# Kernel tuning notes

Measured on AMD Instinct MI355X. Metric: run time of the kernel, lower is better.

The kernel has to match this reference:

```python
import jax, jax.numpy as jnp
import numpy as np

D = 2        # dof (input_dim of fc1)
H1 = 64      # hidden width
N = 262144   # batch
NEG_SLOPE = -0.01  # NOTE: original uses self.neg_slope=-0.01 in the analytic derivative
                   # while the forward activation uses F.leaky_relu default slope +0.01.
                   # We replicate this exactly.

def _lin_init(k, out_d, in_d):
    bound = 1.0 / np.sqrt(in_d)
    kw, kb = jax.random.split(k)
    W = jax.random.uniform(kw, (out_d, in_d), minval=-bound, maxval=bound, dtype=jnp.float32)
    b = jax.random.uniform(kb, (out_d,), minval=-bound, maxval=bound, dtype=jnp.float32)
    return W, b

def setup_inputs():
    key = jax.random.key(0)
    ks = jax.random.split(key, 6)
    W1, b1 = _lin_init(ks[0], H1, D)
    W1a, b1a = _lin_init(ks[1], H1, H1)
    W2, b2 = _lin_init(ks[2], D, H1)
    W3, b3 = _lin_init(ks[3], D, H1)
    W4, b4 = _lin_init(ks[4], 1, H1)
    x = jax.random.normal(ks[5], (N, 3 * D), dtype=jnp.float32)
    return {"x": x, "W1": W1, "b1": b1, "W1a": W1a, "b1a": b1a,
            "W2": W2, "b2": b2, "W3": W3, "b3": b3, "W4": W4, "b4": b4}

def _forward(x, W1, b1, W1a, b1a, W2, b2, W3, b3, W4, b4):
    n = x.shape[0]
    d = x.shape[1] // 3
    q, qd, qdd = x[:, :d], x[:, d:2 * d], x[:, 2 * d:]

    h1 = jax.nn.leaky_relu(q @ W1.T + b1, 0.01)       # [n,H1]
    h2 = jax.nn.leaky_relu(h1 @ W1a.T + b1a, 0.01)    # [n,H1]
    g = h2 @ W2.T + b2                                # [n,d]
    ld = jax.nn.relu(h2 @ W3.T + b3)                  # [n,d]  diagonal of L
    lo = h2 @ W4.T + b4                               # [n,1]  off-diagonal(s)

    # Analytic Jacobians. diag_embed(a) @ W == a[:,:,None] * W (no [n,H,H] materialization).
    dR1 = jnp.where(h1 > 0, 1.0, NEG_SLOPE)
    dh1_dq = dR1[:, :, None] * W1[None]                              # [n,H1,d]
    dR2 = jnp.where(h2 > 0, 1.0, NEG_SLOPE)
    dh2_dq = dR2[:, :, None] * jnp.einsum('hk,nkd->nhd', W1a, dh1_dq)  # [n,H1,d]
    dR3 = jnp.where(ld > 0, 1.0, 0.0)
    dld_dq = dR3[:, :, None] * jnp.einsum('oh,nhd->nod', W3, dh2_dq)   # [n,d,d]
    dlo_dq = jnp.einsum('oh,nhd->nod', W4, dh2_dq)                     # [n,1,d]

    dld_dqi = jnp.transpose(dld_dq, (0, 2, 1))[..., None]  # [n,d,d,1]
    dlo_dqi = jnp.transpose(dlo_dq, (0, 2, 1))[..., None]  # [n,d,1,1]
    dld_dt = dld_dq @ qd[:, :, None]                       # [n,d,1]
    dlo_dt = dlo_dq @ qd[:, :, None]                       # [n,1,1]

    zeros = jnp.zeros_like(ld)
    zeros2 = jnp.zeros_like(dld_dqi)
    Lc, dLt, dLq = [], [], []
    s, e = 0, d - 1
    for i in range(d):  # loop over d (=2) columns of the Cholesky factor
        Lc.append(jnp.concatenate([zeros[:, :i], ld[:, i:i + 1], lo[:, s:e]], axis=1))
        dLt.append(jnp.concatenate([zeros[:, :i], dld_dt[:, i].reshape(n, 1),
                                    dlo_dt[:, s:e].reshape(n, -1)], axis=1))
        dLq.append(jnp.concatenate([zeros2[:, :, :i].reshape(n, d, -1),
                                    dld_dqi[:, :, i].reshape(n, d, 1),
                                    dlo_dqi[:, :, s:e].reshape(n, d, -1)], axis=2))
        s, e = s + e, e + d - 2 - i
    L = jnp.stack(Lc, axis=2)                                    # [n,d,d]
    dL_dt = jnp.stack(dLt, axis=2)                               # [n,d,d]
    dL_dqi = jnp.transpose(jnp.stack(dLq, axis=3), (0, 2, 3, 1)) # [n,d,d,d]

    eps = 1e-5
    Lt = jnp.swapaxes(L, 1, 2)
    Hm = L @ Lt + eps * jnp.eye(d, dtype=x.dtype)
    dH_dt = L @ jnp.swapaxes(dL_dt, 1, 2) + dL_dt @ Lt

    qts = []
    for i in range(d):
        A = dL_dqi[..., i] @ Lt + L @ jnp.swapaxes(dL_dqi[..., i], 1, 2)
        qts.append(qd[:, None, :] @ A @ qd[:, :, None])  # [n,1,1]
    quad = jnp.stack(qts, axis=1).reshape(n, d, 1)

    c = dH_dt @ qd[:, :, None] - 0.5 * quad
    tau = Hm @ qdd[:, :, None] + c + g[:, :, None]
    return tau[..., 0], Hm, c[..., 0], g

def reference(x, W1, b1, W1a, b1a, W2, b2, W3, b3, W4, b4):
    return _forward(x, W1, b1, W1a, b1a, W2, b2, W3, b3, W4, b4)
```

## Files before the change

kernel.cpp:

```cpp
#include <hip/hip_runtime.h>
#include <stdint.h>


typedef __attribute__((ext_vector_type(8))) _Float16 f16x8;
typedef __attribute__((ext_vector_type(4))) float f32x4;
typedef __attribute__((ext_vector_type(2))) float f32x2;
typedef __attribute__((ext_vector_type(4))) unsigned int u32x4;

#define MFMA16(A,B,C) __builtin_amdgcn_mfma_f32_16x16x32_f16((A),(B),(C),0,0,0)

static __device__ __forceinline__ f32x2 pk_fma(f32x2 a, f32x2 b, f32x2 c) {
    f32x2 d;
    asm("v_pk_fma_f32 %0, %1, %2, %3" : "=v"(d) : "v"(a), "v"(b), "v"(c));
    return d;
}
static __device__ __forceinline__ f32x2 pk_mul(f32x2 a, f32x2 b) {
    f32x2 d;
    asm("v_pk_mul_f32 %0, %1, %2" : "=v"(d) : "v"(a), "v"(b));
    return d;
}
static __device__ __forceinline__ unsigned pkmul16(unsigned a, unsigned b) {
    unsigned d;
    asm("v_pk_mul_f16 %0, %1, %2" : "=v"(d) : "v"(a), "v"(b));
    return d;
}
static __device__ __forceinline__ float qsum(float v) {
    float a = v, b = v;
    asm("v_permlane16_swap_b32 %0, %1" : "+v"(a), "+v"(b));
    const float s = a + b;
    float c = s, d = s;
    asm("v_permlane32_swap_b32 %0, %1" : "+v"(c), "+v"(d));
    return c + d;
}

__global__ __launch_bounds__(256, 4) void delan_fwd(
    const float* __restrict__ x,
    const float* __restrict__ W1,  const float* __restrict__ b1,
    const float* __restrict__ W1a, const float* __restrict__ b1a,
    const float* __restrict__ W2,  const float* __restrict__ b2,
    const float* __restrict__ W3,  const float* __restrict__ b3,
    const float* __restrict__ W4,  const float* __restrict__ b4,
    float* __restrict__ out, int n_total)
{
    __shared__ _Float16 afrag[2][4][2][64][8];
    __shared__ float w0s[64], w1s[64], bs[64];
    __shared__ float cst[6][64];

    const int tid  = threadIdx.x;
    const int lane = tid & 63;
    const int wid  = tid >> 6;
    const int p    = lane & 15;
    const int qrt  = lane >> 4;
    const int s    = blockIdx.x * 64 + wid * 16 + p;
    const int sc   = (s < n_total) ? s : (n_total - 1);

    const float2 xa = *(const float2*)(x + 6 * sc);
    const float2 xb = *(const float2*)(x + 6 * sc + 2);
    const float2 xc = *(const float2*)(x + 6 * sc + 4);
    const float x0 = xa.x, x1 = xa.y;
    const float x2 = xb.x, x3 = xb.y;
    const float x4 = xc.x, x5 = xc.y;

    if (tid < 64) {
        const int k = tid;
        w0s[k] = W1[2*k]; w1s[k] = W1[2*k+1]; bs[k] = b1[k];
        cst[0][k] = W2[k];      cst[1][k] = W2[64 + k];
        cst[2][k] = W3[k];      cst[3][k] = W3[64 + k];
        cst[4][k] = W4[k];      cst[5][k] = b1a[k];
    }
    {
        const int ht = wid;
#pragma unroll
        for (int kh = 0; kh < 2; ++kh) {
            const int row = ht * 16 + p;
            const int kb  = kh * 32 + qrt * 8;
            float wv[8];
            *(float4*)&wv[0] = *(const float4*)(W1a + row * 64 + kb);
            *(float4*)&wv[4] = *(const float4*)(W1a + row * 64 + kb + 4);
            f16x8 hi, lo;
#pragma unroll
            for (int j = 0; j < 8; ++j) {
                const _Float16 h = (_Float16)wv[j];
                hi[j] = h;
                lo[j] = (_Float16)((wv[j] - (float)h) * 4096.0f);
            }
            *(f16x8*)&afrag[0][ht][kh][lane][0] = hi;
            *(f16x8*)&afrag[1][ht][kh][lane][0] = lo;
        }
    }
    __syncthreads();

    const f32x2 c4096  = {4096.0f, 4096.0f};
    const f32x2 cm4096 = {-4096.0f, -4096.0f};

    const f32x2 q00 = {x0, x0};
    const f32x2 q11 = {x1, x1};
    u32x4 Bhh[2], Bhl[2], Bu0[2], Bu1[2];
#pragma unroll
    for (int kh = 0; kh < 2; ++kh) {
        const int kb = kh * 32 + qrt * 8;
#pragma unroll
        for (int c = 0; c < 4; ++c) {
            const f32x2 w0p = *(const f32x2*)&w0s[kb + 2*c];
            const f32x2 w1p = *(const f32x2*)&w1s[kb + 2*c];
            const f32x2 bp  = *(const f32x2*)&bs [kb + 2*c];
            const f32x2 prep = pk_fma(w0p, q00, pk_fma(w1p, q11, bp));
            const bool pos0 = prep.x > 0.0f;
            const bool pos1 = prep.y > 0.0f;
            const unsigned mlo = pos0 ? 0x00003C00u : 0x0000A11Fu;
            const unsigned mhi = pos1 ? 0x3C000000u : 0xA11F0000u;
            const unsigned drw = mlo | mhi;
            const unsigned p0w = __builtin_bit_cast(unsigned,
                __builtin_amdgcn_cvt_pkrtz(w0p.x, w0p.y));
            const unsigned p1w = __builtin_bit_cast(unsigned,
                __builtin_amdgcn_cvt_pkrtz(w1p.x, w1p.y));
            Bu0[kh][c] = pkmul16(p0w, drw);
            Bu1[kh][c] = pkmul16(p1w, drw);
            f32x2 sp;
            sp.x = pos0 ? 1.0f : 0.01f;
            sp.y = pos1 ? 1.0f : 0.01f;
            const f32x2 h1p = pk_mul(prep, sp);
            const auto hhv = __builtin_amdgcn_cvt_pkrtz(h1p.x, h1p.y);
            Bhh[kh][c] = __builtin_bit_cast(unsigned, hhv);
            f32x2 hf;
            hf.x = (float)hhv[0];
            hf.y = (float)hhv[1];
            const f32x2 tt = pk_mul(h1p, c4096);
            const f32x2 rp = pk_fma(hf, cm4096, tt);
            Bhl[kh][c] = __builtin_bit_cast(unsigned,
                __builtin_amdgcn_cvt_pkrtz(rp.x, rp.y));
        }
    }

    float ag0=0.f, ag1=0.f, al0=0.f, al1=0.f, aoo=0.f;
    float ap00=0.f, ap01=0.f, ap10=0.f, ap11=0.f, ar0=0.f, ar1=0.f;
#pragma unroll
    for (int ht = 0; ht < 4; ++ht) {
        const f16x8 Ah0 = *(const f16x8*)&afrag[0][ht][0][lane][0];
        const f16x8 Ah1 = *(const f16x8*)&afrag[0][ht][1][lane][0];
        const f16x8 Al0 = *(const f16x8*)&afrag[1][ht][0][lane][0];
        const f16x8 Al1 = *(const f16x8*)&afrag[1][ht][1][lane][0];
        const f16x8 bh0 = __builtin_bit_cast(f16x8, Bhh[0]);
        const f16x8 bh1 = __builtin_bit_cast(f16x8, Bhh[1]);
        const f16x8 bl0 = __builtin_bit_cast(f16x8, Bhl[0]);
        const f16x8 bl1 = __builtin_bit_cast(f16x8, Bhl[1]);
        const f16x8 bu00 = __builtin_bit_cast(f16x8, Bu0[0]);
        const f16x8 bu01 = __builtin_bit_cast(f16x8, Bu0[1]);
        const f16x8 bu10 = __builtin_bit_cast(f16x8, Bu1[0]);
        const f16x8 bu11 = __builtin_bit_cast(f16x8, Bu1[1]);

        const int hb = ht * 16 + qrt * 4;
        f32x4 Chi = *(const f32x4*)&cst[5][hb];
        f32x4 Clo = {0.f,0.f,0.f,0.f};
        f32x4 Cz0 = {0.f,0.f,0.f,0.f};
        f32x4 Cz1 = {0.f,0.f,0.f,0.f};
        Chi = MFMA16(Ah0, bh0, Chi);  Chi = MFMA16(Ah1, bh1, Chi);
        Clo = MFMA16(Ah0, bl0, Clo);  Clo = MFMA16(Ah1, bl1, Clo);
        Clo = MFMA16(Al0, bh0, Clo);  Clo = MFMA16(Al1, bh1, Clo);
        Cz0 = MFMA16(Ah0, bu00, Cz0); Cz0 = MFMA16(Ah1, bu01, Cz0);
        Cz1 = MFMA16(Ah0, bu10, Cz1); Cz1 = MFMA16(Ah1, bu11, Cz1);

        const f32x4 w2a  = *(const f32x4*)&cst[0][hb];
        const f32x4 w2b  = *(const f32x4*)&cst[1][hb];
        const f32x4 w3a  = *(const f32x4*)&cst[2][hb];
        const f32x4 w3b  = *(const f32x4*)&cst[3][hb];
        const f32x4 w4v  = *(const f32x4*)&cst[4][hb];
#pragma unroll
        for (int r = 0; r < 4; ++r) {
            const float ah = fmaf(2.44140625e-4f, Clo[r], Chi[r]);
            const bool pos = ah > 0.0f;
            const float h2 = pos ? ah : 0.01f * ah;
            ag0 = fmaf(w2a[r], h2, ag0);   ag1 = fmaf(w2b[r], h2, ag1);
            al0 = fmaf(w3a[r], h2, al0);   al1 = fmaf(w3b[r], h2, al1);
            aoo = fmaf(w4v[r], h2, aoo);
            const float z0 = Cz0[r], z1 = Cz1[r];
            const float d0 = pos ? z0 : -0.01f * z0;
            const float d1 = pos ? z1 : -0.01f * z1;
            ap00 = fmaf(w3a[r], d0, ap00); ap01 = fmaf(w3a[r], d1, ap01);
            ap10 = fmaf(w3b[r], d0, ap10); ap11 = fmaf(w3b[r], d1, ap11);
            ar0  = fmaf(w4v[r], d0, ar0);  ar1  = fmaf(w4v[r], d1, ar1);
        }
    }

    const float g0 = qsum(ag0) + b2[0];
    const float g1 = qsum(ag1) + b2[1];
    const float l0 = qsum(al0) + b3[0];
    const float l1 = qsum(al1) + b3[1];
    const float oo = qsum(aoo) + b4[0];
    const float p00 = qsum(ap00), p01 = qsum(ap01);
    const float p10 = qsum(ap10), p11 = qsum(ap11);
    const float r0 = qsum(ar0),  r1 = qsum(ar1);

    const float ld0 = fmaxf(l0, 0.0f);
    const float ld1 = fmaxf(l1, 0.0f);
    const float dr30 = (l0 > 0.0f) ? 1.0f : 0.0f;
    const float dr31 = (l1 > 0.0f) ? 1.0f : 0.0f;

    const float da00 = dr30 * p00, da01 = dr30 * p01;
    const float da10 = dr31 * p10, da11 = dr31 * p11;

    const float l00 = ld0, l10 = oo, l11 = ld1;

    const float m00 = da00 * x2 + da01 * x3;
    const float m11 = da10 * x2 + da11 * x3;
    const float m10 = r0  * x2 + r1  * x3;

    const float eps = 1e-5f;
    const float Hm00 = fmaf(l00, l00, eps);
    const float Hm01 = l00 * l10;
    const float Hm11 = fmaf(l10, l10, fmaf(l11, l11, eps));

    const float dH00 = 2.0f * l00 * m00;
    const float dH01 = fmaf(l00, m10, l10 * m00);
    const float dH11 = 2.0f * fmaf(l10, m10, l11 * m11);

    const float x22 = x2 * x2, x23 = x2 * x3, x33 = x3 * x3;
    const float quad0 = 2.0f * (da00 * l00 * x22
                      + (fmaf(da00, l10, r0 * l00)) * x23
                      + (fmaf(r0, l10, da10 * l11)) * x33);
    const float quad1 = 2.0f * (da01 * l00 * x22
                      + (fmaf(da01, l10, r1 * l00)) * x23
                      + (fmaf(r1, l10, da11 * l11)) * x33);

    const float c0 = fmaf(dH00, x2, dH01 * x3) - 0.5f * quad0;
    const float c1 = fmaf(dH01, x2, dH11 * x3) - 0.5f * quad1;

    const float tau0 = fmaf(Hm00, x4, Hm01 * x5) + c0 + g0;
    const float tau1 = fmaf(Hm01, x4, Hm11 * x5) + c1 + g1;

    if (s < n_total) {
        const long long N = n_total;
        if (qrt == 0) {
            *((float2*)out + s) = make_float2(tau0, tau1);
        } else if (qrt == 1) {
            *((float4*)(out + 2 * N) + s) = make_float4(Hm00, Hm01, Hm01, Hm11);
        } else if (qrt == 2) {
            *((float2*)(out + 6 * N) + s) = make_float2(c0, c1);
        } else {
            *((float2*)(out + 8 * N) + s) = make_float2(g0, g1);
        }
    }
}

extern "C" void kernel_launch(void* const* d_in, const int* in_sizes, int n_in,
                              void* d_out, int out_size, void* d_ws, size_t ws_size,
                              hipStream_t stream) {
    const float* x   = (const float*)d_in[0];
    const float* W1  = (const float*)d_in[1];
    const float* b1  = (const float*)d_in[2];
    const float* W1a = (const float*)d_in[3];
    const float* b1a = (const float*)d_in[4];
    const float* W2  = (const float*)d_in[5];
    const float* b2  = (const float*)d_in[6];
    const float* W3  = (const float*)d_in[7];
    const float* b3  = (const float*)d_in[8];
    const float* W4  = (const float*)d_in[9];
    const float* b4  = (const float*)d_in[10];
    float* out = (float*)d_out;

    const int n_total = in_sizes[0] / 6;
    const int block = 256;
    const int grid = (n_total + 63) / 64;
    delan_fwd<<<grid, block, 0, stream>>>(x, W1, b1, W1a, b1a, W2, b2,
                                          W3, b3, W4, b4, out, n_total);
}
```

Before: 30.60 us.

## Switch to 32x32x16 MFMA with 32 samples per wave

Replaces the 16x16x32 MFMA tiling (16 samples per wave, 4 lane groups) with 32x32x16 MFMA so each wave handles 32 samples. Per-sample work is replicated across 2 lane groups instead of 4, which cuts the redundant per-lane epilogue work and allows a single permlane32 reduction. Small weight vectors now come straight from global memory instead of LDS, and each block covers twice the samples. In exchange the kernel uses more accumulator registers, so launch bounds drop to 3 blocks per CU.

```diff
diff --git a/kernel.cpp b/kernel.cpp
--- a/kernel.cpp
+++ b/kernel.cpp
@@ -3,11 +3,11 @@
 
 
 typedef __attribute__((ext_vector_type(8))) _Float16 f16x8;
-typedef __attribute__((ext_vector_type(4))) float f32x4;
+typedef __attribute__((ext_vector_type(16))) float f32x16;
 typedef __attribute__((ext_vector_type(2))) float f32x2;
 typedef __attribute__((ext_vector_type(4))) unsigned int u32x4;
 
-#define MFMA16(A,B,C) __builtin_amdgcn_mfma_f32_16x16x32_f16((A),(B),(C),0,0,0)
+#define MFMA32(A,B,C) __builtin_amdgcn_mfma_f32_32x32x16_f16((A),(B),(C),0,0,0)
 
 static __device__ __forceinline__ f32x2 pk_fma(f32x2 a, f32x2 b, f32x2 c) {
     f32x2 d;
@@ -24,16 +24,13 @@
     asm("v_pk_mul_f16 %0, %1, %2" : "=v"(d) : "v"(a), "v"(b));
     return d;
 }
-static __device__ __forceinline__ float qsum(float v) {
+static __device__ __forceinline__ float hsum32(float v) {
     float a = v, b = v;
-    asm("v_permlane16_swap_b32 %0, %1" : "+v"(a), "+v"(b));
-    const float s = a + b;
-    float c = s, d = s;
-    asm("v_permlane32_swap_b32 %0, %1" : "+v"(c), "+v"(d));
-    return c + d;
-}
-
-__global__ __launch_bounds__(256, 4) void delan_fwd(
+    asm("v_permlane32_swap_b32 %0, %1" : "+v"(a), "+v"(b));
+    return a + b;
+}
+
+__global__ __launch_bounds__(256, 3) void delan_fwd(
     const float* __restrict__ x,
     const float* __restrict__ W1,  const float* __restrict__ b1,
     const float* __restrict__ W1a, const float* __restrict__ b1a,
@@ -42,16 +39,14 @@
     const float* __restrict__ W4,  const float* __restrict__ b4,
     float* __restrict__ out, int n_total)
 {
-    __shared__ _Float16 afrag[2][4][2][64][8];
-    __shared__ float w0s[64], w1s[64], bs[64];
-    __shared__ float cst[6][64];
+    __shared__ _Float16 ahl[2][2][4][64][8];
 
     const int tid  = threadIdx.x;
     const int lane = tid & 63;
     const int wid  = tid >> 6;
-    const int p    = lane & 15;
-    const int qrt  = lane >> 4;
-    const int s    = blockIdx.x * 64 + wid * 16 + p;
+    const int col  = lane & 31;
+    const int g    = lane >> 5;
+    const int s    = blockIdx.x * 128 + wid * 32 + col;
     const int sc   = (s < n_total) ? s : (n_total - 1);
 
     const float2 xa = *(const float2*)(x + 6 * sc);
@@ -61,49 +56,46 @@
     const float x2 = xb.x, x3 = xb.y;
     const float x4 = xc.x, x5 = xc.y;
 
-    if (tid < 64) {
-        const int k = tid;
-        w0s[k] = W1[2*k]; w1s[k] = W1[2*k+1]; bs[k] = b1[k];
-        cst[0][k] = W2[k];      cst[1][k] = W2[64 + k];
-        cst[2][k] = W3[k];      cst[3][k] = W3[64 + k];
-        cst[4][k] = W4[k];      cst[5][k] = b1a[k];
-    }
-    {
-        const int ht = wid;
-#pragma unroll
-        for (int kh = 0; kh < 2; ++kh) {
-            const int row = ht * 16 + p;
-            const int kb  = kh * 32 + qrt * 8;
-            float wv[8];
-            *(float4*)&wv[0] = *(const float4*)(W1a + row * 64 + kb);
-            *(float4*)&wv[4] = *(const float4*)(W1a + row * 64 + kb + 4);
-            f16x8 hi, lo;
-#pragma unroll
-            for (int j = 0; j < 8; ++j) {
-                const _Float16 h = (_Float16)wv[j];
-                hi[j] = h;
-                lo[j] = (_Float16)((wv[j] - (float)h) * 4096.0f);
-            }
-            *(f16x8*)&afrag[0][ht][kh][lane][0] = hi;
-            *(f16x8*)&afrag[1][ht][kh][lane][0] = lo;
-        }
+#pragma unroll
+    for (int i = 0; i < 2; ++i) {
+        const int combo = wid * 2 + i;
+        const int H = combo >> 2;
+        const int b = combo & 3;
+        const int row = 32 * H + col;
+        const int ks  = 16 * b + 8 * g;
+        const float4 a0 = *(const float4*)(W1a + row * 64 + ks);
+        const float4 a1 = *(const float4*)(W1a + row * 64 + ks + 4);
+        const float v[8] = {a0.x, a0.y, a0.z, a0.w, a1.x, a1.y, a1.z, a1.w};
+        f16x8 hi, lo;
+#pragma unroll
+        for (int j = 0; j < 8; ++j) {
+            const _Float16 h = (_Float16)v[j];
+            hi[j] = h;
+            lo[j] = (_Float16)((v[j] - (float)h) * 4096.0f);
+        }
+        *(f16x8*)&ahl[0][H][b][lane][0] = hi;
+        *(f16x8*)&ahl[1][H][b][lane][0] = lo;
     }
     __syncthreads();
 
+    const f32x2 q00 = {x0, x0};
+    const f32x2 q11 = {x1, x1};
     const f32x2 c4096  = {4096.0f, 4096.0f};
     const f32x2 cm4096 = {-4096.0f, -4096.0f};
-
-    const f32x2 q00 = {x0, x0};
-    const f32x2 q11 = {x1, x1};
-    u32x4 Bhh[2], Bhl[2], Bu0[2], Bu1[2];
-#pragma unroll
-    for (int kh = 0; kh < 2; ++kh) {
-        const int kb = kh * 32 + qrt * 8;
+    u32x4 Bhh[4], Bhl[4], Bu0[4], Bu1[4];
+#pragma unroll
+    for (int b = 0; b < 4; ++b) {
+        const int kb = 16 * b + 8 * g;
+        const float4* wq = (const float4*)(W1 + 2 * kb);
+        const float4 bq0 = *(const float4*)(b1 + kb);
+        const float4 bq1 = *(const float4*)(b1 + kb + 4);
+        const float bv[8] = {bq0.x, bq0.y, bq0.z, bq0.w, bq1.x, bq1.y, bq1.z, bq1.w};
 #pragma unroll
         for (int c = 0; c < 4; ++c) {
-            const f32x2 w0p = *(const f32x2*)&w0s[kb + 2*c];
-            const f32x2 w1p = *(const f32x2*)&w1s[kb + 2*c];
-            const f32x2 bp  = *(const f32x2*)&bs [kb + 2*c];
+            const float4 w = wq[c];
+            const f32x2 w0p = {w.x, w.z};
+            const f32x2 w1p = {w.y, w.w};
+            const f32x2 bp  = {bv[2*c], bv[2*c+1]};
             const f32x2 prep = pk_fma(w0p, q00, pk_fma(w1p, q11, bp));
             const bool pos0 = prep.x > 0.0f;
             const bool pos1 = prep.y > 0.0f;
@@ -114,20 +106,20 @@
                 __builtin_amdgcn_cvt_pkrtz(w0p.x, w0p.y));
             const unsigned p1w = __builtin_bit_cast(unsigned,
                 __builtin_amdgcn_cvt_pkrtz(w1p.x, w1p.y));
-            Bu0[kh][c] = pkmul16(p0w, drw);
-            Bu1[kh][c] = pkmul16(p1w, drw);
+            Bu0[b][c] = pkmul16(p0w, drw);
+            Bu1[b][c] = pkmul16(p1w, drw);
             f32x2 sp;
             sp.x = pos0 ? 1.0f : 0.01f;
             sp.y = pos1 ? 1.0f : 0.01f;
             const f32x2 h1p = pk_mul(prep, sp);
             const auto hhv = __builtin_amdgcn_cvt_pkrtz(h1p.x, h1p.y);
-            Bhh[kh][c] = __builtin_bit_cast(unsigned, hhv);
+            Bhh[b][c] = __builtin_bit_cast(unsigned, hhv);
             f32x2 hf;
             hf.x = (float)hhv[0];
             hf.y = (float)hhv[1];
             const f32x2 tt = pk_mul(h1p, c4096);
             const f32x2 rp = pk_fma(hf, cm4096, tt);
-            Bhl[kh][c] = __builtin_bit_cast(unsigned,
+            Bhl[b][c] = __builtin_bit_cast(unsigned,
                 __builtin_amdgcn_cvt_pkrtz(rp.x, rp.y));
         }
     }
@@ -135,61 +127,80 @@
     float ag0=0.f, ag1=0.f, al0=0.f, al1=0.f, aoo=0.f;
     float ap00=0.f, ap01=0.f, ap10=0.f, ap11=0.f, ar0=0.f, ar1=0.f;
 #pragma unroll
-    for (int ht = 0; ht < 4; ++ht) {
-        const f16x8 Ah0 = *(const f16x8*)&afrag[0][ht][0][lane][0];
-        const f16x8 Ah1 = *(const f16x8*)&afrag[0][ht][1][lane][0];
-        const f16x8 Al0 = *(const f16x8*)&afrag[1][ht][0][lane][0];
-        const f16x8 Al1 = *(const f16x8*)&afrag[1][ht][1][lane][0];
-        const f16x8 bh0 = __builtin_bit_cast(f16x8, Bhh[0]);
-        const f16x8 bh1 = __builtin_bit_cast(f16x8, Bhh[1]);
-        const f16x8 bl0 = __builtin_bit_cast(f16x8, Bhl[0]);
-        const f16x8 bl1 = __builtin_bit_cast(f16x8, Bhl[1]);
-        const f16x8 bu00 = __builtin_bit_cast(f16x8, Bu0[0]);
-        const f16x8 bu01 = __builtin_bit_cast(f16x8, Bu0[1]);
-        const f16x8 bu10 = __builtin_bit_cast(f16x8, Bu1[0]);
-        const f16x8 bu11 = __builtin_bit_cast(f16x8, Bu1[1]);
-
-        const int hb = ht * 16 + qrt * 4;
-        f32x4 Chi = *(const f32x4*)&cst[5][hb];
-        f32x4 Clo = {0.f,0.f,0.f,0.f};
-        f32x4 Cz0 = {0.f,0.f,0.f,0.f};
-        f32x4 Cz1 = {0.f,0.f,0.f,0.f};
-        Chi = MFMA16(Ah0, bh0, Chi);  Chi = MFMA16(Ah1, bh1, Chi);
-        Clo = MFMA16(Ah0, bl0, Clo);  Clo = MFMA16(Ah1, bl1, Clo);
-        Clo = MFMA16(Al0, bh0, Clo);  Clo = MFMA16(Al1, bh1, Clo);
-        Cz0 = MFMA16(Ah0, bu00, Cz0); Cz0 = MFMA16(Ah1, bu01, Cz0);
-        Cz1 = MFMA16(Ah0, bu10, Cz1); Cz1 = MFMA16(Ah1, bu11, Cz1);
-
-        const f32x4 w2a  = *(const f32x4*)&cst[0][hb];
-        const f32x4 w2b  = *(const f32x4*)&cst[1][hb];
-        const f32x4 w3a  = *(const f32x4*)&cst[2][hb];
-        const f32x4 w3b  = *(const f32x4*)&cst[3][hb];
-        const f32x4 w4v  = *(const f32x4*)&cst[4][hb];
-#pragma unroll
-        for (int r = 0; r < 4; ++r) {
+    for (int H = 0; H < 2; ++H) {
+        f16x8 Ah[4], Al[4];
+#pragma unroll
+        for (int b = 0; b < 4; ++b) {
+            Ah[b] = *(const f16x8*)&ahl[0][H][b][lane][0];
+            Al[b] = *(const f16x8*)&ahl[1][H][b][lane][0];
+        }
+#define BB(arr, b) __builtin_bit_cast(f16x8, arr[b])
+        f32x16 Chi;
+#pragma unroll
+        for (int rq = 0; rq < 4; ++rq) {
+            const float4 bq = *(const float4*)(b1a + 32*H + 8*rq + 4*g);
+            Chi[4*rq+0] = bq.x; Chi[4*rq+1] = bq.y;
+            Chi[4*rq+2] = bq.z; Chi[4*rq+3] = bq.w;
+        }
+#pragma unroll
+        for (int b = 0; b < 4; ++b) Chi = MFMA32(Ah[b], BB(Bhh,b), Chi);
+        f32x16 Clo = {0.f};
+#pragma unroll
+        for (int b = 0; b < 4; ++b) Clo = MFMA32(Ah[b], BB(Bhl,b), Clo);
+#pragma unroll
+        for (int b = 0; b < 4; ++b) Clo = MFMA32(Al[b], BB(Bhh,b), Clo);
+        float h2v[16];
+#pragma unroll
+        for (int r = 0; r < 16; ++r) {
             const float ah = fmaf(2.44140625e-4f, Clo[r], Chi[r]);
-            const bool pos = ah > 0.0f;
-            const float h2 = pos ? ah : 0.01f * ah;
-            ag0 = fmaf(w2a[r], h2, ag0);   ag1 = fmaf(w2b[r], h2, ag1);
-            al0 = fmaf(w3a[r], h2, al0);   al1 = fmaf(w3b[r], h2, al1);
-            aoo = fmaf(w4v[r], h2, aoo);
-            const float z0 = Cz0[r], z1 = Cz1[r];
-            const float d0 = pos ? z0 : -0.01f * z0;
-            const float d1 = pos ? z1 : -0.01f * z1;
-            ap00 = fmaf(w3a[r], d0, ap00); ap01 = fmaf(w3a[r], d1, ap01);
-            ap10 = fmaf(w3b[r], d0, ap10); ap11 = fmaf(w3b[r], d1, ap11);
-            ar0  = fmaf(w4v[r], d0, ar0);  ar1  = fmaf(w4v[r], d1, ar1);
-        }
-    }
-
-    const float g0 = qsum(ag0) + b2[0];
-    const float g1 = qsum(ag1) + b2[1];
-    const float l0 = qsum(al0) + b3[0];
-    const float l1 = qsum(al1) + b3[1];
-    const float oo = qsum(aoo) + b4[0];
-    const float p00 = qsum(ap00), p01 = qsum(ap01);
-    const float p10 = qsum(ap10), p11 = qsum(ap11);
-    const float r0 = qsum(ar0),  r1 = qsum(ar1);
+            h2v[r] = (ah > 0.0f) ? ah : 0.01f * ah;
+        }
+        f32x16 Cz0 = {0.f};
+        f32x16 Cz1 = {0.f};
+#pragma unroll
+        for (int b = 0; b < 4; ++b) Cz0 = MFMA32(Ah[b], BB(Bu0,b), Cz0);
+#pragma unroll
+        for (int b = 0; b < 4; ++b) Cz1 = MFMA32(Ah[b], BB(Bu1,b), Cz1);
+#undef BB
+#pragma unroll
+        for (int rq = 0; rq < 4; ++rq) {
+            const int hb = 32*H + 8*rq + 4*g;
+            const float4 w2a = *(const float4*)(W2 + hb);
+            const float4 w2b = *(const float4*)(W2 + 64 + hb);
+            const float4 w3a = *(const float4*)(W3 + hb);
+            const float4 w3b = *(const float4*)(W3 + 64 + hb);
+            const float4 w4v = *(const float4*)(W4 + hb);
+            const float w2av[4] = {w2a.x, w2a.y, w2a.z, w2a.w};
+            const float w2bv[4] = {w2b.x, w2b.y, w2b.z, w2b.w};
+            const float w3av[4] = {w3a.x, w3a.y, w3a.z, w3a.w};
+            const float w3bv[4] = {w3b.x, w3b.y, w3b.z, w3b.w};
+            const float w4vv[4] = {w4v.x, w4v.y, w4v.z, w4v.w};
+#pragma unroll
+            for (int rr = 0; rr < 4; ++rr) {
+                const int r = 4*rq + rr;
+                const float h2 = h2v[r];
+                const bool pos = h2 > 0.0f;
+                ag0 = fmaf(w2av[rr], h2, ag0);   ag1 = fmaf(w2bv[rr], h2, ag1);
+                al0 = fmaf(w3av[rr], h2, al0);   al1 = fmaf(w3bv[rr], h2, al1);
+                aoo = fmaf(w4vv[rr], h2, aoo);
+                const float z0 = Cz0[r], z1 = Cz1[r];
+                const float d0 = pos ? z0 : -0.01f * z0;
+                const float d1 = pos ? z1 : -0.01f * z1;
+                ap00 = fmaf(w3av[rr], d0, ap00); ap01 = fmaf(w3av[rr], d1, ap01);
+                ap10 = fmaf(w3bv[rr], d0, ap10); ap11 = fmaf(w3bv[rr], d1, ap11);
+                ar0  = fmaf(w4vv[rr], d0, ar0);  ar1  = fmaf(w4vv[rr], d1, ar1);
+            }
+        }
+    }
+
+    const float g0 = hsum32(ag0) + b2[0];
+    const float g1 = hsum32(ag1) + b2[1];
+    const float l0 = hsum32(al0) + b3[0];
+    const float l1 = hsum32(al1) + b3[1];
+    const float oo = hsum32(aoo) + b4[0];
+    const float p00 = hsum32(ap00), p01 = hsum32(ap01);
+    const float p10 = hsum32(ap10), p11 = hsum32(ap11);
+    const float r0 = hsum32(ar0),  r1 = hsum32(ar1);
 
     const float ld0 = fmaxf(l0, 0.0f);
     const float ld1 = fmaxf(l1, 0.0f);
@@ -230,13 +241,11 @@
 
     if (s < n_total) {
         const long long N = n_total;
-        if (qrt == 0) {
+        if (g == 0) {
             *((float2*)out + s) = make_float2(tau0, tau1);
-        } else if (qrt == 1) {
             *((float4*)(out + 2 * N) + s) = make_float4(Hm00, Hm01, Hm01, Hm11);
-        } else if (qrt == 2) {
+        } else {
             *((float2*)(out + 6 * N) + s) = make_float2(c0, c1);
-        } else {
             *((float2*)(out + 8 * N) + s) = make_float2(g0, g1);
         }
     }
@@ -260,7 +269,7 @@
 
     const int n_total = in_sizes[0] / 6;
     const int block = 256;
-    const int grid = (n_total + 63) / 64;
+    const int grid = (n_total + 127) / 128;
     delan_fwd<<<grid, block, 0, stream>>>(x, W1, b1, W1a, b1a, W2, b2,
                                           W3, b3, W4, b4, out, n_total);
 }
```

New measurement: 32.60 us. +6.5%, slower.
